# Performance work log

Hardware: AMD Instinct MI355X
Metric: run time of the kernel (lower is better)

Reference implementation:

```python
import jax, jax.numpy as jnp
import numpy as np

OUT_F, IN_F = 4096, 11008
NUMEL = OUT_F * IN_F            # divisible by 256
NUM_SUPER = NUMEL // 256        # super-blocks of 8 sub-blocks x 32 values


def setup_inputs() -> dict:
    key = jax.random.key(0)
    k = jax.random.split(key, 7)
    x = jax.random.normal(k[0], (64, IN_F), dtype=jnp.float32)
    packed = jax.random.randint(k[1], (NUMEL // 2,), 0, 256, dtype=jnp.int32)
    d = jax.random.uniform(k[2], (NUM_SUPER,), dtype=jnp.float32) * 0.02
    dmin = jax.random.uniform(k[3], (NUM_SUPER,), dtype=jnp.float32) * 0.02
    scales = jax.random.randint(k[4], (NUM_SUPER * 8,), 0, 64, dtype=jnp.int32)
    mins = jax.random.randint(k[5], (NUM_SUPER * 8,), 0, 64, dtype=jnp.int32)
    bias = jax.random.normal(k[6], (OUT_F,), dtype=jnp.float32) * 0.02
    return {"x": x, "packed": packed, "d": d, "dmin": dmin,
            "scales": scales, "mins": mins, "bias": bias}


def _dequant_q4k(packed, d, dmin, scales, mins):
    # unpack two 4-bit quants per byte, interleaved low/high (stack dim=1 + flatten)
    low = packed & 15
    high = (packed >> 4) & 15
    q = jnp.stack([low, high], axis=1).reshape(NUM_SUPER, 8, 32).astype(jnp.float32)
    sc = (scales.astype(jnp.float32) / 63.0).reshape(NUM_SUPER, 8, 1)
    mn = (mins.astype(jnp.float32) / 63.0).reshape(NUM_SUPER, 8, 1)
    normalized = q / 15.0 * sc + mn
    w = normalized * d.reshape(NUM_SUPER, 1, 1) + dmin.reshape(NUM_SUPER, 1, 1)
    return w.reshape(OUT_F, IN_F)


def reference(x, packed, d, dmin, scales, mins, bias):
    w = _dequant_q4k(packed, d, dmin, scales, mins)   # [OUT_F, IN_F] fp32
    return x @ w.T + bias                              # F.linear
```

## Files before the change

kernel.cpp:

```cpp
#include <hip/hip_runtime.h>
#include <stdint.h>

#define OUT_F   4096
#define IN_F    11008
#define BATCH   64
#define NSUP    43
#define SB_ROW  344
#define IPR     5504
#define NKS     16
#define XP_BYTES   (4 * 344 * 64 * 16)
#define PART_ELEMS ((size_t)NKS * BATCH * OUT_F)
#define WS_FULL    (XP_BYTES + PART_ELEMS * 4)

typedef __attribute__((ext_vector_type(8))) short  short8;
typedef __attribute__((ext_vector_type(4))) float  floatx4;
typedef __attribute__((ext_vector_type(4))) int    intx4;

__device__ __forceinline__ unsigned pack_bf16(float f0, float f1) {
    return __builtin_amdgcn_perm(__float_as_uint(f1), __float_as_uint(f0), 0x07060302u);
}

__global__ __launch_bounds__(256) void xprep_kernel(const float* __restrict__ x,
                                                    intx4* __restrict__ xp) {
    const int ksb = blockIdx.x;
    const int mt  = threadIdx.x >> 6;
    const int l   = threadIdx.x & 63;
    const int lo  = l & 15, hi = l >> 4;
    const float* src = x + (mt * 16 + lo) * IN_F + ksb * 32 + hi * 8;
    floatx4 a0 = *(const floatx4*)src;
    floatx4 a1 = *(const floatx4*)(src + 4);
    intx4 r;
    r.x = pack_bf16(a0.x, a0.y);
    r.y = pack_bf16(a0.z, a0.w);
    r.z = pack_bf16(a1.x, a1.y);
    r.w = pack_bf16(a1.z, a1.w);
    xp[(mt * 344 + ksb) * 64 + l] = r;
}

__global__ __launch_bounds__(256) void init_out_kernel(const float* __restrict__ bias,
                                                       float* __restrict__ out) {
    int i = blockIdx.x * 256 + threadIdx.x;
    out[i] = bias[i & (OUT_F - 1)];
}

__global__ __launch_bounds__(256) void reduce_kernel(const float* __restrict__ part,
                                                     const float* __restrict__ bias,
                                                     float* __restrict__ out) {
    const int i = blockIdx.x * 256 + threadIdx.x;
    float s = bias[i & (OUT_F - 1)];
    #pragma unroll
    for (int k = 0; k < NKS; ++k) s += part[(size_t)k * (BATCH * OUT_F) + i];
    out[i] = s;
}

template<bool USE_PART>
__global__ __launch_bounds__(256, 2) void qlin_main(
    const intx4* __restrict__ xp,
    const int*   __restrict__ packed,
    const float* __restrict__ dd,
    const float* __restrict__ dmn_g,
    const int*   __restrict__ scales,
    const int*   __restrict__ mins,
    float*       __restrict__ part,
    float*       __restrict__ out)
{
    const int ks = blockIdx.x & 15;
    const int nb = blockIdx.x >> 4;
    const int w  = threadIdx.x >> 6;
    const int l  = threadIdx.x & 63;
    const int lo = l & 15, hi = l >> 4;

    const int o    = nb * 64 + w * 16 + lo;
    const int sup0 = ks < 11 ? 3 * ks : 33 + 2 * (ks - 11);
    const int nsup = ks < 11 ? 3 : 2;

    const int*   bp0  = packed + o * IPR + sup0 * 128 + hi * 4;
    const intx4* xq0  = xp + (sup0 * 8) * 64 + l;
    const int*   scp0 = scales + o * SB_ROW + sup0 * 8;
    const int*   mnp0 = mins   + o * SB_ROW + sup0 * 8;
    const int    didx0 = o * NSUP + sup0;

    floatx4 acc[4];
    #pragma unroll
    for (int mt = 0; mt < 4; ++mt) acc[mt] = (floatx4)0.0f;

    #pragma unroll 1
    for (int s = 0; s < nsup; ++s) {
        const int*   bp = bp0 + s * 128;
        const intx4* xq = xq0 + s * 512;

        intx4 br[8];
        #pragma unroll
        for (int st = 0; st < 8; ++st)
            br[st] = __builtin_nontemporal_load((const intx4*)(bp + st * 16));

        intx4 xf[32];
        #pragma unroll
        for (int mt = 0; mt < 4; ++mt) {
            #pragma unroll
            for (int st = 0; st < 8; ++st)
                xf[mt * 8 + st] = xq[(mt * 344 + st) * 64];
        }

        const intx4 sc0 = *(const intx4*)(scp0 + s * 8);
        const intx4 sc1 = *(const intx4*)(scp0 + s * 8 + 4);
        const intx4 mn0 = *(const intx4*)(mnp0 + s * 8);
        const intx4 mn1 = *(const intx4*)(mnp0 + s * 8 + 4);
        const float dv  = dd[didx0 + s];
        const float dmv = dmn_g[didx0 + s];
        const float A945 = dv * (1.0f / 945.0f);
        const float A63  = dv * (1.0f / 63.0f);

        #pragma unroll
        for (int st = 0; st < 8; ++st) {
            const int scv = (st < 4) ? sc0[st & 3] : sc1[st & 3];
            const int mnv = (st < 4) ? mn0[st & 3] : mn1[st & 3];
            const float A = A945 * (float)scv;
            const float B = fmaf(A63, (float)mnv, dmv);
            const int v0 = br[st].x, v1 = br[st].y, v2 = br[st].z, v3 = br[st].w;
            union { intx4 i; short8 s8; } uw;
            uw.i.x = pack_bf16(fmaf((float)(v0 & 15), A, B), fmaf((float)(v0 >> 4), A, B));
            uw.i.y = pack_bf16(fmaf((float)(v1 & 15), A, B), fmaf((float)(v1 >> 4), A, B));
            uw.i.z = pack_bf16(fmaf((float)(v2 & 15), A, B), fmaf((float)(v2 >> 4), A, B));
            uw.i.w = pack_bf16(fmaf((float)(v3 & 15), A, B), fmaf((float)(v3 >> 4), A, B));

            union { intx4 i; short8 s8; } u0, u1, u2, u3;
            u0.i = xf[0 * 8 + st];
            u1.i = xf[1 * 8 + st];
            u2.i = xf[2 * 8 + st];
            u3.i = xf[3 * 8 + st];
            acc[0] = __builtin_amdgcn_mfma_f32_16x16x32_bf16(u0.s8, uw.s8, acc[0], 0, 0, 0);
            acc[1] = __builtin_amdgcn_mfma_f32_16x16x32_bf16(u1.s8, uw.s8, acc[1], 0, 0, 0);
            acc[2] = __builtin_amdgcn_mfma_f32_16x16x32_bf16(u2.s8, uw.s8, acc[2], 0, 0, 0);
            acc[3] = __builtin_amdgcn_mfma_f32_16x16x32_bf16(u3.s8, uw.s8, acc[3], 0, 0, 0);
        }
    }

    if (USE_PART) {
        float* pbase = part + (size_t)ks * (BATCH * OUT_F) + o;
        #pragma unroll
        for (int mt = 0; mt < 4; ++mt) {
            #pragma unroll
            for (int r = 0; r < 4; ++r)
                pbase[(mt * 16 + hi * 4 + r) * OUT_F] = acc[mt][r];
        }
    } else {
        #pragma unroll
        for (int mt = 0; mt < 4; ++mt) {
            #pragma unroll
            for (int r = 0; r < 4; ++r)
                atomicAdd(out + (mt * 16 + hi * 4 + r) * OUT_F + o, acc[mt][r]);
        }
    }
}

extern "C" void kernel_launch(void* const* d_in, const int* in_sizes, int n_in,
                              void* d_out, int out_size, void* d_ws, size_t ws_size,
                              hipStream_t stream) {
    (void)in_sizes; (void)n_in; (void)out_size;
    const float* x      = (const float*)d_in[0];
    const int*   packed = (const int*)d_in[1];
    const float* d      = (const float*)d_in[2];
    const float* dmin   = (const float*)d_in[3];
    const int*   scales = (const int*)d_in[4];
    const int*   mins   = (const int*)d_in[5];
    const float* bias   = (const float*)d_in[6];
    float* out = (float*)d_out;

    const bool has_part = ws_size >= (size_t)WS_FULL;
    intx4* xp   = (intx4*)d_ws;
    float* part = (float*)((char*)d_ws + XP_BYTES);

    xprep_kernel<<<344, 256, 0, stream>>>(x, xp);

    if (has_part) {
        qlin_main<true><<<64 * NKS, 256, 0, stream>>>(
            xp, packed, d, dmin, scales, mins, part, out);
        reduce_kernel<<<(BATCH * OUT_F) / 256, 256, 0, stream>>>(part, bias, out);
    } else {
        init_out_kernel<<<(BATCH * OUT_F) / 256, 256, 0, stream>>>(bias, out);
        qlin_main<false><<<64 * NKS, 256, 0, stream>>>(
            xp, packed, d, dmin, scales, mins, part, out);
    }
}
```

Measured before the change: 181.3 us.

## Stage activations and scale metadata in LDS, cut K-splits to twelve

Each block now loads the bf16 activation tile for its super-block once, cooperatively, into shared memory. Waves then read their MFMA operands from LDS instead of each fetching all 32 fragments from global memory. Scales, mins, d and dmin are likewise loaded coalesced by one wave each and shared through LDS. The K split drops from 16 to 12, with 3-4 super-blocks per block, which shrinks the partial-sum buffer and the reduce traffic. Block order is changed so neighbouring blocks share a K slice, and occupancy is raised to 3 blocks per SIMD. The cost is two barriers per iteration and about 36KB of LDS per block, which may limit occupancy.

New measurement: 167.7 us. -7.6%, faster.

```diff
diff --git a/kernel.cpp b/kernel.cpp
--- a/kernel.cpp
+++ b/kernel.cpp
@@ -7,7 +7,7 @@
 #define NSUP    43
 #define SB_ROW  344
 #define IPR     5504
-#define NKS     16
+#define NKS     12
 #define XP_BYTES   (4 * 344 * 64 * 16)
 #define PART_ELEMS ((size_t)NKS * BATCH * OUT_F)
 #define WS_FULL    (XP_BYTES + PART_ELEMS * 4)
@@ -54,7 +54,7 @@
 }
 
 template<bool USE_PART>
-__global__ __launch_bounds__(256, 2) void qlin_main(
+__global__ __launch_bounds__(256, 3) void qlin_main(
     const intx4* __restrict__ xp,
     const int*   __restrict__ packed,
     const float* __restrict__ dd,
@@ -64,57 +64,92 @@
     float*       __restrict__ part,
     float*       __restrict__ out)
 {
-    const int ks = blockIdx.x & 15;
-    const int nb = blockIdx.x >> 4;
-    const int w  = threadIdx.x >> 6;
-    const int l  = threadIdx.x & 63;
-    const int lo = l & 15, hi = l >> 4;
+    __shared__ intx4 xfs[2048];
+    __shared__ int   scs[512];
+    __shared__ int   mns[512];
+    __shared__ float dsx[64];
+    __shared__ float dmx[64];
+
+    const int nb  = blockIdx.x & 63;
+    const int ks  = blockIdx.x >> 6;
+    const int tid = threadIdx.x;
+    const int w   = tid >> 6;
+    const int l   = tid & 63;
+    const int lo  = l & 15, hi = l >> 4;
 
     const int o    = nb * 64 + w * 16 + lo;
-    const int sup0 = ks < 11 ? 3 * ks : 33 + 2 * (ks - 11);
-    const int nsup = ks < 11 ? 3 : 2;
-
-    const int*   bp0  = packed + o * IPR + sup0 * 128 + hi * 4;
-    const intx4* xq0  = xp + (sup0 * 8) * 64 + l;
-    const int*   scp0 = scales + o * SB_ROW + sup0 * 8;
-    const int*   mnp0 = mins   + o * SB_ROW + sup0 * 8;
-    const int    didx0 = o * NSUP + sup0;
+    const int r    = w * 16 + lo;
+    const int sup0 = ks < 7 ? 4 * ks : 28 + 3 * (ks - 7);
+    const int nsup = ks < 7 ? 4 : 3;
 
     floatx4 acc[4];
     #pragma unroll
     for (int mt = 0; mt < 4; ++mt) acc[mt] = (floatx4)0.0f;
 
+    const int* bp0 = packed + o * IPR + sup0 * 128 + hi * 4;
+    const int tr = tid & 63;
+    const int og = nb * 64 + tr;
+
     #pragma unroll 1
     for (int s = 0; s < nsup; ++s) {
-        const int*   bp = bp0 + s * 128;
-        const intx4* xq = xq0 + s * 512;
+        const int sup = sup0 + s;
 
         intx4 br[8];
         #pragma unroll
         for (int st = 0; st < 8; ++st)
-            br[st] = __builtin_nontemporal_load((const intx4*)(bp + st * 16));
-
-        intx4 xf[32];
-        #pragma unroll
-        for (int mt = 0; mt < 4; ++mt) {
-            #pragma unroll
-            for (int st = 0; st < 8; ++st)
-                xf[mt * 8 + st] = xq[(mt * 344 + st) * 64];
-        }
-
-        const intx4 sc0 = *(const intx4*)(scp0 + s * 8);
-        const intx4 sc1 = *(const intx4*)(scp0 + s * 8 + 4);
-        const intx4 mn0 = *(const intx4*)(mnp0 + s * 8);
-        const intx4 mn1 = *(const intx4*)(mnp0 + s * 8 + 4);
-        const float dv  = dd[didx0 + s];
-        const float dmv = dmn_g[didx0 + s];
+            br[st] = __builtin_nontemporal_load((const intx4*)(bp0 + s * 128 + st * 16));
+
+        intx4 xtmp[8];
+        const intx4* xsrc = xp + sup * 512;
+        #pragma unroll
+        for (int i = 0; i < 8; ++i) {
+            const int idx = i * 256 + tid;
+            xtmp[i] = xsrc[(idx >> 9) * 22016 + (idx & 511)];
+        }
+        intx4 sct0, sct1;
+        float dtmp = 0.0f;
+        if (w == 0) {
+            sct0 = *(const intx4*)(scales + og * SB_ROW + sup * 8);
+            sct1 = *(const intx4*)(scales + og * SB_ROW + sup * 8 + 4);
+        } else if (w == 1) {
+            sct0 = *(const intx4*)(mins + og * SB_ROW + sup * 8);
+            sct1 = *(const intx4*)(mins + og * SB_ROW + sup * 8 + 4);
+        } else if (w == 2) {
+            dtmp = dd[og * NSUP + sup];
+        } else {
+            dtmp = dmn_g[og * NSUP + sup];
+        }
+
+        if (s > 0) __syncthreads();
+        #pragma unroll
+        for (int i = 0; i < 8; ++i)
+            xfs[i * 256 + tid] = xtmp[i];
+        if (w == 0) {
+            *(intx4*)&scs[tr * 8]     = sct0;
+            *(intx4*)&scs[tr * 8 + 4] = sct1;
+        } else if (w == 1) {
+            *(intx4*)&mns[tr * 8]     = sct0;
+            *(intx4*)&mns[tr * 8 + 4] = sct1;
+        } else if (w == 2) {
+            dsx[tr] = dtmp;
+        } else {
+            dmx[tr] = dtmp;
+        }
+        __syncthreads();
+
+        const float dv   = dsx[r];
+        const float dmv  = dmx[r];
         const float A945 = dv * (1.0f / 945.0f);
         const float A63  = dv * (1.0f / 63.0f);
+        const intx4 s0 = *(const intx4*)&scs[r * 8];
+        const intx4 s1 = *(const intx4*)&scs[r * 8 + 4];
+        const intx4 m0 = *(const intx4*)&mns[r * 8];
+        const intx4 m1 = *(const intx4*)&mns[r * 8 + 4];
 
         #pragma unroll
         for (int st = 0; st < 8; ++st) {
-            const int scv = (st < 4) ? sc0[st & 3] : sc1[st & 3];
-            const int mnv = (st < 4) ? mn0[st & 3] : mn1[st & 3];
+            const int scv = (st < 4) ? s0[st & 3] : s1[st & 3];
+            const int mnv = (st < 4) ? m0[st & 3] : m1[st & 3];
             const float A = A945 * (float)scv;
             const float B = fmaf(A63, (float)mnv, dmv);
             const int v0 = br[st].x, v1 = br[st].y, v2 = br[st].z, v3 = br[st].w;
@@ -125,10 +160,10 @@
             uw.i.w = pack_bf16(fmaf((float)(v3 & 15), A, B), fmaf((float)(v3 >> 4), A, B));
 
             union { intx4 i; short8 s8; } u0, u1, u2, u3;
-            u0.i = xf[0 * 8 + st];
-            u1.i = xf[1 * 8 + st];
-            u2.i = xf[2 * 8 + st];
-            u3.i = xf[3 * 8 + st];
+            u0.i = xfs[0 * 512 + st * 64 + l];
+            u1.i = xfs[1 * 512 + st * 64 + l];
+            u2.i = xfs[2 * 512 + st * 64 + l];
+            u3.i = xfs[3 * 512 + st * 64 + l];
             acc[0] = __builtin_amdgcn_mfma_f32_16x16x32_bf16(u0.s8, uw.s8, acc[0], 0, 0, 0);
             acc[1] = __builtin_amdgcn_mfma_f32_16x16x32_bf16(u1.s8, uw.s8, acc[1], 0, 0, 0);
             acc[2] = __builtin_amdgcn_mfma_f32_16x16x32_bf16(u2.s8, uw.s8, acc[2], 0, 0, 0);
@@ -141,15 +176,15 @@
         #pragma unroll
         for (int mt = 0; mt < 4; ++mt) {
             #pragma unroll
-            for (int r = 0; r < 4; ++r)
-                pbase[(mt * 16 + hi * 4 + r) * OUT_F] = acc[mt][r];
+            for (int rr = 0; rr < 4; ++rr)
+                pbase[(mt * 16 + hi * 4 + rr) * OUT_F] = acc[mt][rr];
         }
     } else {
         #pragma unroll
         for (int mt = 0; mt < 4; ++mt) {
             #pragma unroll
-            for (int r = 0; r < 4; ++r)
-                atomicAdd(out + (mt * 16 + hi * 4 + r) * OUT_F + o, acc[mt][r]);
+            for (int rr = 0; rr < 4; ++rr)
+                atomicAdd(out + (mt * 16 + hi * 4 + rr) * OUT_F + o, acc[mt][rr]);
         }
     }
 }
```

## Stage activations in LDS with double buffering and widen output tile per block

Applied to the files above, without the earlier changes.

Each block now covers 128 output rows instead of 64, with two 16-column tiles per wave. Activation fragments are staged through double-buffered shared memory, so each block reads them from global memory once and all four waves share them. A new prep kernel packs the scales and mins into bytes and transposes them, along with d and dmin, into a per-super-block layout so they can be loaded coalesced. Packed weight loads are split into halves and prefetched one super-block ahead. The trade-off is half as many blocks (512), an extra kernel launch, more registers, and syncthreads overhead.

Result: faster. 168.2 us (-7.2%).

```diff
diff --git a/kernel.cpp b/kernel.cpp
--- a/kernel.cpp
+++ b/kernel.cpp
@@ -8,9 +8,13 @@
 #define SB_ROW  344
 #define IPR     5504
 #define NKS     16
-#define XP_BYTES   (4 * 344 * 64 * 16)
-#define PART_ELEMS ((size_t)NKS * BATCH * OUT_F)
-#define WS_FULL    (XP_BYTES + PART_ELEMS * 4)
+#define NCB     32
+#define XP_BYTES   (344 * 256 * 16)
+#define SCMN_BYTES (NSUP * 4096 * 16)
+#define DDM_BYTES  (NSUP * 4096 * 8)
+#define PART_OFF   (XP_BYTES + SCMN_BYTES + DDM_BYTES)
+#define PART_BYTES ((size_t)NKS * BATCH * OUT_F * 4)
+#define WS_FULL    (PART_OFF + PART_BYTES)
 
 typedef __attribute__((ext_vector_type(8))) short  short8;
 typedef __attribute__((ext_vector_type(4))) float  floatx4;
@@ -37,6 +41,31 @@
     xp[(mt * 344 + ksb) * 64 + l] = r;
 }
 
+__global__ __launch_bounds__(256) void scprep_kernel(const int* __restrict__ scales,
+                                                     const int* __restrict__ mins,
+                                                     const float* __restrict__ dd,
+                                                     const float* __restrict__ dmn,
+                                                     intx4* __restrict__ scmn_p,
+                                                     float2* __restrict__ ddm_p) {
+    const int tg  = blockIdx.x * 256 + threadIdx.x;
+    const int row = tg / 43;
+    const int sup = tg - row * 43;
+    const intx4 s0 = *(const intx4*)(scales + row * SB_ROW + sup * 8);
+    const intx4 s1 = *(const intx4*)(scales + row * SB_ROW + sup * 8 + 4);
+    const intx4 m0 = *(const intx4*)(mins   + row * SB_ROW + sup * 8);
+    const intx4 m1 = *(const intx4*)(mins   + row * SB_ROW + sup * 8 + 4);
+    intx4 o;
+    o.x = s0.x | (s0.y << 8) | (s0.z << 16) | (s0.w << 24);
+    o.y = s1.x | (s1.y << 8) | (s1.z << 16) | (s1.w << 24);
+    o.z = m0.x | (m0.y << 8) | (m0.z << 16) | (m0.w << 24);
+    o.w = m1.x | (m1.y << 8) | (m1.z << 16) | (m1.w << 24);
+    scmn_p[sup * 4096 + row] = o;
+    float2 dp;
+    dp.x = dd[row * NSUP + sup];
+    dp.y = dmn[row * NSUP + sup];
+    ddm_p[sup * 4096 + row] = dp;
+}
+
 __global__ __launch_bounds__(256) void init_out_kernel(const float* __restrict__ bias,
                                                        float* __restrict__ out) {
     int i = blockIdx.x * 256 + threadIdx.x;
@@ -55,101 +84,153 @@
 
 template<bool USE_PART>
 __global__ __launch_bounds__(256, 2) void qlin_main(
-    const intx4* __restrict__ xp,
-    const int*   __restrict__ packed,
-    const float* __restrict__ dd,
-    const float* __restrict__ dmn_g,
-    const int*   __restrict__ scales,
-    const int*   __restrict__ mins,
-    float*       __restrict__ part,
-    float*       __restrict__ out)
+    const intx4*  __restrict__ xp,
+    const int*    __restrict__ packed,
+    const intx4*  __restrict__ scmn_p,
+    const float2* __restrict__ ddm_p,
+    float*        __restrict__ part,
+    float*        __restrict__ out)
 {
-    const int ks = blockIdx.x & 15;
-    const int nb = blockIdx.x >> 4;
-    const int w  = threadIdx.x >> 6;
-    const int l  = threadIdx.x & 63;
-    const int lo = l & 15, hi = l >> 4;
-
-    const int o    = nb * 64 + w * 16 + lo;
+    __shared__ intx4  xfs[2][2048];
+    __shared__ intx4  scs[2][128];
+    __shared__ float2 dds[2][128];
+
+    const int ks  = blockIdx.x & 15;
+    const int nb  = blockIdx.x >> 4;
+    const int tid = threadIdx.x;
+    const int w   = tid >> 6;
+    const int l   = tid & 63;
+    const int lo  = l & 15, hi = l >> 4;
+
     const int sup0 = ks < 11 ? 3 * ks : 33 + 2 * (ks - 11);
     const int nsup = ks < 11 ? 3 : 2;
 
-    const int*   bp0  = packed + o * IPR + sup0 * 128 + hi * 4;
-    const intx4* xq0  = xp + (sup0 * 8) * 64 + l;
-    const int*   scp0 = scales + o * SB_ROW + sup0 * 8;
-    const int*   mnp0 = mins   + o * SB_ROW + sup0 * 8;
-    const int    didx0 = o * NSUP + sup0;
-
-    floatx4 acc[4];
+    const int o0 = nb * 128 + (2 * w) * 16 + lo;
+    const int o1 = o0 + 16;
+    const int* bpA0 = packed + o0 * IPR + hi * 4;
+    const int* bpA1 = packed + o1 * IPR + hi * 4;
+
+    floatx4 acc[4][2];
     #pragma unroll
-    for (int mt = 0; mt < 4; ++mt) acc[mt] = (floatx4)0.0f;
+    for (int mt = 0; mt < 4; ++mt) { acc[mt][0] = (floatx4)0.0f; acc[mt][1] = (floatx4)0.0f; }
+
+    intx4 xtmp[8]; intx4 sctv; float2 ddv;
+
+    auto stage_issue = [&](int sup) {
+        const intx4* xsrc = xp + sup * 512;
+        #pragma unroll
+        for (int i = 0; i < 8; ++i) {
+            const int idx = i * 256 + tid;
+            xtmp[i] = xsrc[(idx >> 9) * 22016 + (idx & 511)];
+        }
+        if (tid < 128) sctv = scmn_p[sup * 4096 + nb * 128 + tid];
+        else           ddv  = ddm_p[sup * 4096 + nb * 128 + (tid - 128)];
+    };
+    auto stage_commit = [&](int b) {
+        #pragma unroll
+        for (int i = 0; i < 8; ++i) xfs[b][i * 256 + tid] = xtmp[i];
+        if (tid < 128) scs[b][tid] = sctv;
+        else           dds[b][tid - 128] = ddv;
+    };
+
+    struct Half { intx4 v[2][4]; };
+    auto load_half = [&](int sup, int half) {
+        Half r;
+        #pragma unroll
+        for (int st = 0; st < 4; ++st) {
+            r.v[0][st] = __builtin_nontemporal_load(
+                (const intx4*)(bpA0 + sup * 128 + half * 64 + st * 16));
+            r.v[1][st] = __builtin_nontemporal_load(
+                (const intx4*)(bpA1 + sup * 128 + half * 64 + st * 16));
+        }
+        return r;
+    };
+
+    Half brP = load_half(sup0, 0);
+    stage_issue(sup0);
+    stage_commit(0);
 
     #pragma unroll 1
     for (int s = 0; s < nsup; ++s) {
-        const int*   bp = bp0 + s * 128;
-        const intx4* xq = xq0 + s * 512;
-
-        intx4 br[8];
-        #pragma unroll
-        for (int st = 0; st < 8; ++st)
-            br[st] = __builtin_nontemporal_load((const intx4*)(bp + st * 16));
-
-        intx4 xf[32];
+        const int b = s & 1;
+        const int sup = sup0 + s;
+        __syncthreads();
+
+        if (s + 1 < nsup) stage_issue(sup + 1);
+        Half brQ = load_half(sup, 1);
+        Half brPn;
+        if (s + 1 < nsup) brPn = load_half(sup + 1, 0);
+
+        const intx4  sv0 = scs[b][w * 32 + lo];
+        const intx4  sv1 = scs[b][w * 32 + 16 + lo];
+        const float2 dp0 = dds[b][w * 32 + lo];
+        const float2 dp1 = dds[b][w * 32 + 16 + lo];
+        const float a945_0 = dp0.x * (1.0f / 945.0f), a63_0 = dp0.x * (1.0f / 63.0f);
+        const float a945_1 = dp1.x * (1.0f / 945.0f), a63_1 = dp1.x * (1.0f / 63.0f);
+
+        auto compute_half = [&](int half, const Half& br) {
+            #pragma unroll
+            for (int st = 0; st < 4; ++st) {
+                const int step = half * 4 + st;
+                intx4 x0 = xfs[b][0 * 512 + step * 64 + l];
+                intx4 x1 = xfs[b][1 * 512 + step * 64 + l];
+                intx4 x2 = xfs[b][2 * 512 + step * 64 + l];
+                intx4 x3 = xfs[b][3 * 512 + step * 64 + l];
+                #pragma unroll
+                for (int nt = 0; nt < 2; ++nt) {
+                    const intx4 sv = nt ? sv1 : sv0;
+                    const int scw = half ? sv.y : sv.x;
+                    const int mnw = half ? sv.w : sv.z;
+                    const float A = (nt ? a945_1 : a945_0) * (float)((scw >> (st * 8)) & 255);
+                    const float B = fmaf((nt ? a63_1 : a63_0),
+                                         (float)((mnw >> (st * 8)) & 255),
+                                         (nt ? dp1.y : dp0.y));
+                    const intx4 bv = br.v[nt][st];
+                    union { intx4 i; short8 s8; } uw;
+                    uw.i.x = pack_bf16(fmaf((float)(bv.x & 15), A, B),
+                                       fmaf((float)(bv.x >> 4), A, B));
+                    uw.i.y = pack_bf16(fmaf((float)(bv.y & 15), A, B),
+                                       fmaf((float)(bv.y >> 4), A, B));
+                    uw.i.z = pack_bf16(fmaf((float)(bv.z & 15), A, B),
+                                       fmaf((float)(bv.z >> 4), A, B));
+                    uw.i.w = pack_bf16(fmaf((float)(bv.w & 15), A, B),
+                                       fmaf((float)(bv.w >> 4), A, B));
+                    union { intx4 i; short8 s8; } u0, u1, u2, u3;
+                    u0.i = x0; u1.i = x1; u2.i = x2; u3.i = x3;
+                    acc[0][nt] = __builtin_amdgcn_mfma_f32_16x16x32_bf16(u0.s8, uw.s8, acc[0][nt], 0, 0, 0);
+                    acc[1][nt] = __builtin_amdgcn_mfma_f32_16x16x32_bf16(u1.s8, uw.s8, acc[1][nt], 0, 0, 0);
+                    acc[2][nt] = __builtin_amdgcn_mfma_f32_16x16x32_bf16(u2.s8, uw.s8, acc[2][nt], 0, 0, 0);
+                    acc[3][nt] = __builtin_amdgcn_mfma_f32_16x16x32_bf16(u3.s8, uw.s8, acc[3][nt], 0, 0, 0);
+                }
+            }
+        };
+
+        compute_half(0, brP);
+        compute_half(1, brQ);
+
+        if (s + 1 < nsup) { stage_commit(1 - b); brP = brPn; }
+    }
+
+    if (USE_PART) {
+        float* p0 = part + (size_t)ks * (BATCH * OUT_F);
         #pragma unroll
         for (int mt = 0; mt < 4; ++mt) {
             #pragma unroll
-            for (int st = 0; st < 8; ++st)
-                xf[mt * 8 + st] = xq[(mt * 344 + st) * 64];
-        }
-
-        const intx4 sc0 = *(const intx4*)(scp0 + s * 8);
-        const intx4 sc1 = *(const intx4*)(scp0 + s * 8 + 4);
-        const intx4 mn0 = *(const intx4*)(mnp0 + s * 8);
-        const intx4 mn1 = *(const intx4*)(mnp0 + s * 8 + 4);
-        const float dv  = dd[didx0 + s];
-        const float dmv = dmn_g[didx0 + s];
-        const float A945 = dv * (1.0f / 945.0f);
-        const float A63  = dv * (1.0f / 63.0f);
-
-        #pragma unroll
-        for (int st = 0; st < 8; ++st) {
-            const int scv = (st < 4) ? sc0[st & 3] : sc1[st & 3];
-            const int mnv = (st < 4) ? mn0[st & 3] : mn1[st & 3];
-            const float A = A945 * (float)scv;
-            const float B = fmaf(A63, (float)mnv, dmv);
-            const int v0 = br[st].x, v1 = br[st].y, v2 = br[st].z, v3 = br[st].w;
-            union { intx4 i; short8 s8; } uw;
-            uw.i.x = pack_bf16(fmaf((float)(v0 & 15), A, B), fmaf((float)(v0 >> 4), A, B));
-            uw.i.y = pack_bf16(fmaf((float)(v1 & 15), A, B), fmaf((float)(v1 >> 4), A, B));
-            uw.i.z = pack_bf16(fmaf((float)(v2 & 15), A, B), fmaf((float)(v2 >> 4), A, B));
-            uw.i.w = pack_bf16(fmaf((float)(v3 & 15), A, B), fmaf((float)(v3 >> 4), A, B));
-
-            union { intx4 i; short8 s8; } u0, u1, u2, u3;
-            u0.i = xf[0 * 8 + st];
-            u1.i = xf[1 * 8 + st];
-            u2.i = xf[2 * 8 + st];
-            u3.i = xf[3 * 8 + st];
-            acc[0] = __builtin_amdgcn_mfma_f32_16x16x32_bf16(u0.s8, uw.s8, acc[0], 0, 0, 0);
-            acc[1] = __builtin_amdgcn_mfma_f32_16x16x32_bf16(u1.s8, uw.s8, acc[1], 0, 0, 0);
-            acc[2] = __builtin_amdgcn_mfma_f32_16x16x32_bf16(u2.s8, uw.s8, acc[2], 0, 0, 0);
-            acc[3] = __builtin_amdgcn_mfma_f32_16x16x32_bf16(u3.s8, uw.s8, acc[3], 0, 0, 0);
-        }
-    }
-
-    if (USE_PART) {
-        float* pbase = part + (size_t)ks * (BATCH * OUT_F) + o;
+            for (int r = 0; r < 4; ++r) {
+                const int row = (mt * 16 + hi * 4 + r) * OUT_F;
+                p0[row + o0] = acc[mt][0][r];
+                p0[row + o1] = acc[mt][1][r];
+            }
+        }
+    } else {
         #pragma unroll
         for (int mt = 0; mt < 4; ++mt) {
             #pragma unroll
-            for (int r = 0; r < 4; ++r)
-                pbase[(mt * 16 + hi * 4 + r) * OUT_F] = acc[mt][r];
-        }
-    } else {
-        #pragma unroll
-        for (int mt = 0; mt < 4; ++mt) {
-            #pragma unroll
-            for (int r = 0; r < 4; ++r)
-                atomicAdd(out + (mt * 16 + hi * 4 + r) * OUT_F + o, acc[mt][r]);
+            for (int r = 0; r < 4; ++r) {
+                const int row = (mt * 16 + hi * 4 + r) * OUT_F;
+                atomicAdd(out + row + o0, acc[mt][0][r]);
+                atomicAdd(out + row + o1, acc[mt][1][r]);
+            }
         }
     }
 }
@@ -167,19 +248,22 @@
     const float* bias   = (const float*)d_in[6];
     float* out = (float*)d_out;
 
+    intx4*  xp     = (intx4*)d_ws;
+    intx4*  scmn_p = (intx4*)((char*)d_ws + XP_BYTES);
+    float2* ddm_p  = (float2*)((char*)d_ws + XP_BYTES + SCMN_BYTES);
+    float*  part   = (float*)((char*)d_ws + PART_OFF);
     const bool has_part = ws_size >= (size_t)WS_FULL;
-    intx4* xp   = (intx4*)d_ws;
-    float* part = (float*)((char*)d_ws + XP_BYTES);
 
     xprep_kernel<<<344, 256, 0, stream>>>(x, xp);
+    scprep_kernel<<<688, 256, 0, stream>>>(scales, mins, d, dmin, scmn_p, ddm_p);
 
     if (has_part) {
-        qlin_main<true><<<64 * NKS, 256, 0, stream>>>(
-            xp, packed, d, dmin, scales, mins, part, out);
+        qlin_main<true><<<NCB * NKS, 256, 0, stream>>>(
+            xp, packed, scmn_p, ddm_p, part, out);
         reduce_kernel<<<(BATCH * OUT_F) / 256, 256, 0, stream>>>(part, bias, out);
     } else {
         init_out_kernel<<<(BATCH * OUT_F) / 256, 256, 0, stream>>>(bias, out);
-        qlin_main<false><<<64 * NKS, 256, 0, stream>>>(
-            xp, packed, d, dmin, scales, mins, part, out);
+        qlin_main<false><<<NCB * NKS, 256, 0, stream>>>(
+            xp, packed, scmn_p, ddm_p, part, out);
     }
 }
```
